# Optimization experiments

Hardware: AMD Instinct MI355X
Metric: run time of the kernel (lower is better)

The kernel has to match this reference:

```python
import jax, jax.numpy as jnp
import numpy as np

B, C, H, W = 4, 256, 64, 64
G = 32          # GroupNorm groups
KH = KW = 3     # deformable kernel
K = KH * KW
EPS = 1e-5
PAD = 1
DIL = 1
STRIDE = 1


def conv3x3(x, w, b):
    # plain 3x3 conv, stride 1, pad 1 (offset-prediction conv)
    y = jax.lax.conv_general_dilated(
        x, w, window_strides=(1, 1), padding=((1, 1), (1, 1)),
        dimension_numbers=('NCHW', 'OIHW', 'NCHW'))
    return y + b[None, :, None, None]


def group_norm(x, gamma, beta):
    b, c, h, w = x.shape
    xr = x.reshape(b, G, -1)
    mu = jnp.mean(xr, axis=-1, keepdims=True)
    var = jnp.var(xr, axis=-1, keepdims=True)
    xn = ((xr - mu) * jax.lax.rsqrt(var + EPS)).reshape(b, c, h, w)
    return xn * gamma[None, :, None, None] + beta[None, :, None, None]


def deform_conv(x, offset, weight):
    # x: [B,Cin,H,W]; offset: [B,2*K,H,W] as (dy,dx) pairs per kernel tap;
    # weight: [Cout,Cin,KH,KW]. DeformConv v1, no bias, stride=1, pad=1.
    b, cin, h, w = x.shape
    cout = weight.shape[0]
    off = offset.reshape(b, K, 2, h, w)
    dy, dx = off[:, :, 0], off[:, :, 1]          # [B,K,H,W]

    ky = (jnp.arange(K) // KW).astype(x.dtype)   # kernel tap row
    kx = (jnp.arange(K) % KW).astype(x.dtype)    # kernel tap col
    hh = jnp.arange(h, dtype=x.dtype)
    ww = jnp.arange(w, dtype=x.dtype)

    # fractional sampling coordinates, shape [B,K,H,W]
    py = dy + hh[None, None, :, None] * STRIDE - PAD + ky[None, :, None, None] * DIL
    px = dx + ww[None, None, None, :] * STRIDE - PAD + kx[None, :, None, None] * DIL

    y0 = jnp.floor(py)
    x0 = jnp.floor(px)
    ly = py - y0   # bilinear fractions
    lx = px - x0

    xf = x.reshape(b, cin, h * w)

    def gather(yi, xi):
        valid = ((yi >= 0) & (yi < h) & (xi >= 0) & (xi < w)).astype(x.dtype)
        yc = jnp.clip(yi, 0, h - 1).astype(jnp.int32)
        xc = jnp.clip(xi, 0, w - 1).astype(jnp.int32)
        idx = (yc * w + xc).reshape(b, 1, K * h * w)
        g = jnp.take_along_axis(xf, idx, axis=2).reshape(b, cin, K, h, w)
        return g * valid[:, None]

    # accumulate 4 bilinear corners -> sampled patches [B,Cin,K,H,W]
    val = gather(y0, x0) * ((1 - ly) * (1 - lx))[:, None]
    val = val + gather(y0, x0 + 1) * ((1 - ly) * lx)[:, None]
    val = val + gather(y0 + 1, x0) * (ly * (1 - lx))[:, None]
    val = val + gather(y0 + 1, x0 + 1) * (ly * lx)[:, None]

    wk = weight.reshape(cout, cin, K)
    return jnp.einsum('bckhw,ock->bohw', val, wk)


def setup_inputs() -> dict:
    key = jax.random.key(0)
    ks = jax.random.split(key, 12)
    fan = 1.0 / np.sqrt(C * K)
    off_scale = 0.01  # small offsets -> near-grid sampling, as after training-time zero-init
    return {
        'x':      jax.random.normal(ks[0], (B, C, H, W), jnp.float32),
        'w_off1': jax.random.normal(ks[1], (2 * K, C, KH, KW), jnp.float32) * off_scale,
        'b_off1': jnp.zeros((2 * K,), jnp.float32),
        'w_off2': jax.random.normal(ks[2], (2 * K, C, KH, KW), jnp.float32) * off_scale,
        'b_off2': jnp.zeros((2 * K,), jnp.float32),
        'w_def1': jax.random.normal(ks[3], (C, C, KH, KW), jnp.float32) * fan,
        'w_def2': jax.random.normal(ks[4], (C, C, KH, KW), jnp.float32) * fan,
        'gamma1': jnp.ones((C,), jnp.float32),
        'beta1':  jnp.zeros((C,), jnp.float32),
        'gamma2': jnp.ones((C,), jnp.float32),
        'beta2':  jnp.zeros((C,), jnp.float32),
    }


def reference(x, w_off1, b_off1, w_off2, b_off2, w_def1, w_def2,
              gamma1, beta1, gamma2, beta2):
    residual = x
    offset = conv3x3(x, w_off1, b_off1)
    out = deform_conv(x, offset, w_def1)
    out = jax.nn.relu(group_norm(out, gamma1, beta1))
    offset2 = conv3x3(out, w_off2, b_off2)
    out = deform_conv(out, offset2, w_def2)
    out = group_norm(out, gamma2, beta2)
    out = jax.nn.relu(out + residual)
    return out
```

## Files before the change

### kernel.cpp

```cpp
#include <hip/hip_runtime.h>
#include <hip/hip_bf16.h>

typedef unsigned int uint;
typedef unsigned short ushort;
typedef __attribute__((ext_vector_type(8))) short bfrag_t;
typedef __attribute__((ext_vector_type(4))) short s4_t;
typedef __attribute__((ext_vector_type(4))) float f4_t;
typedef __attribute__((ext_vector_type(2))) float f2_t;

#define EPSV 1e-5f

__device__ __forceinline__ float4 ld4(const float* p) { return *(const float4*)p; }
__device__ __forceinline__ void st4(float* p, float4 v) { *(float4*)p = v; }

__device__ __forceinline__ ushort f2bf(float f) {
    union { float f; uint u; } v; v.f = f;
    uint r = v.u + 0x7fffu + ((v.u >> 16) & 1u);
    return (ushort)(r >> 16);
}
__device__ __forceinline__ float bf2f(ushort s) {
    union { uint u; float f; } v; v.u = ((uint)s) << 16;
    return v.f;
}
__device__ __forceinline__ float bfhi(uint u) { union { uint u; float f; } v; v.u = u & 0xffff0000u; return v.f; }
__device__ __forceinline__ float bflo(uint u) { union { uint u; float f; } v; v.u = u << 16; return v.f; }
__device__ __forceinline__ uint pk2(float a, float b) { return (uint)f2bf(a) | ((uint)f2bf(b) << 16); }
__device__ __forceinline__ uint pkrn(float a, float b) {
    union { __hip_bfloat162 h; uint u; } v;
    v.h = __float22bfloat162_rn(make_float2(a, b));
    return v.u;
}

__global__ __launch_bounds__(256) void prep_all(const float* __restrict__ wd1, const float* __restrict__ wd2,
                                                const float* __restrict__ wo1, const float* __restrict__ wo2,
                                                const float* __restrict__ x,
                                                ushort* __restrict__ oT1, ushort* __restrict__ oT2,
                                                ushort* __restrict__ oO1, ushort* __restrict__ oO2,
                                                ushort* __restrict__ xb, float* __restrict__ gnacc) {
    __shared__ float lds[64][65];
    int bid = blockIdx.x;
    int tid = threadIdx.x;
    if (bid < 512) {
        int co = bid & 255;
        int sel = bid >> 8;
        const float* w = sel ? wd2 : wd1;
        ushort* o = sel ? oT2 : oT1;
        const float* p = w + (co * 256 + tid) * 9;
        float v[9];
#pragma unroll
        for (int k = 0; k < 9; ++k) v[k] = p[k];
#pragma unroll
        for (int k = 0; k < 9; ++k) o[(k * 256 + co) * 256 + tid] = f2bf(v[k]);
    } else if (bid < 576) {
        int idx = bid - 512;
        int co = idx & 31;
        int sel = idx >> 5;
        const float* w = sel ? wo2 : wo1;
        ushort* o = sel ? oO2 : oO1;
        float v[9] = {0.f,0.f,0.f,0.f,0.f,0.f,0.f,0.f,0.f};
        if (co < 18) {
            const float* p = w + (co * 256 + tid) * 9;
#pragma unroll
            for (int k = 0; k < 9; ++k) v[k] = p[k];
        }
#pragma unroll
        for (int k = 0; k < 9; ++k) o[(k * 32 + co) * 256 + tid] = f2bf(v[k]);
        if (idx == 0) { gnacc[tid] = 0.f; gnacc[256 + tid] = 0.f; }
    } else {
        int b2 = bid - 576;
        int cb = b2 & 3, y = (b2 >> 2) & 63, b = b2 >> 8;
        int c0 = cb << 6;
#pragma unroll
        for (int i = 0; i < 4; ++i) {
            int q = tid + (i << 8);
            int c_l = q >> 4, x4 = (q & 15) << 2;
            float4 v = ld4(&x[((b * 256 + c0 + c_l) << 12) + (y << 6) + x4]);
            lds[c_l][x4 + 0] = v.x; lds[c_l][x4 + 1] = v.y; lds[c_l][x4 + 2] = v.z; lds[c_l][x4 + 3] = v.w;
        }
        __syncthreads();
#pragma unroll
        for (int i = 0; i < 4; ++i) {
            int q = tid + (i << 8);
            int x_l = q >> 4, c4 = (q & 15) << 2;
            s4_t v;
            v.x = (short)f2bf(lds[c4 + 0][x_l]); v.y = (short)f2bf(lds[c4 + 1][x_l]);
            v.z = (short)f2bf(lds[c4 + 2][x_l]); v.w = (short)f2bf(lds[c4 + 3][x_l]);
            *(s4_t*)&xb[(((b << 12) + (y << 6) + x_l) << 8) + c0 + c4] = v;
        }
    }
}

template<int FUSE>
__global__ __launch_bounds__(512, 2) void offconv8(const ushort* __restrict__ xb, const float* __restrict__ gnacc,
                                                   const float* __restrict__ gamma, const float* __restrict__ beta,
                                                   const ushort* __restrict__ wO,
                                                   const float* __restrict__ bias, float* __restrict__ offb) {
    __shared__ float red2[8][64][33];
    int bidx = blockIdx.x;
    int tile = (bidx & 7) * 32 + (bidx >> 3);
    int px0 = tile << 6;
    int b = tile >> 6;
    int y = tile & 63;
    int tid = threadIdx.x;
    int wave = tid >> 6, lane = tid & 63;
    int lr = lane & 15, lq = lane >> 4;
    int cio = (wave << 5) + (lq << 3);

    float s8[8], t8[8];
    if (FUSE) {
        int g = cio >> 3;
        float2 a = *(const float2*)(gnacc + ((b << 5) + g) * 2);
        float mean = a.x * (1.f / 32768.f);
        float var = fmaxf(a.y * (1.f / 32768.f) - mean * mean, 0.f);
        float rstd = rsqrtf(var + EPSV);
#pragma unroll
        for (int j = 0; j < 8; ++j) {
            float ga = gamma[cio + j];
            s8[j] = ga * rstd;
            t8[j] = beta[cio + j] - mean * s8[j];
        }
    }

    f4_t acc[4][2];
#pragma unroll
    for (int m = 0; m < 4; ++m)
#pragma unroll
        for (int n = 0; n < 2; ++n) acc[m][n] = (f4_t){0.f,0.f,0.f,0.f};

#pragma unroll
    for (int tap = 0; tap < 9; ++tap) {
        int ky = tap / 3, kx = tap - ky * 3;
        int yy = y + ky - 1;
        if ((uint)yy < 64u) {
            const ushort* wrow = wO + ((tap << 5) << 8) + cio;
            bfrag_t b0 = *(const bfrag_t*)(wrow + (lr << 8));
            bfrag_t b1 = *(const bfrag_t*)(wrow + ((16 + lr) << 8));
            const ushort* arow = xb + (((b << 6) + yy) << 14) + cio;
#pragma unroll
            for (int m = 0; m < 4; ++m) {
                int xx = (m << 4) + lr + kx - 1;
                bfrag_t afr = (bfrag_t){0,0,0,0,0,0,0,0};
                if ((uint)xx < 64u) {
                    if (FUSE) {
                        uint4 raw = *(const uint4*)(arow + (xx << 8));
                        union { uint4 u; bfrag_t f; } cv;
                        cv.u.x = pkrn(fmaxf(s8[0]*bflo(raw.x)+t8[0], 0.f), fmaxf(s8[1]*bfhi(raw.x)+t8[1], 0.f));
                        cv.u.y = pkrn(fmaxf(s8[2]*bflo(raw.y)+t8[2], 0.f), fmaxf(s8[3]*bfhi(raw.y)+t8[3], 0.f));
                        cv.u.z = pkrn(fmaxf(s8[4]*bflo(raw.z)+t8[4], 0.f), fmaxf(s8[5]*bfhi(raw.z)+t8[5], 0.f));
                        cv.u.w = pkrn(fmaxf(s8[6]*bflo(raw.w)+t8[6], 0.f), fmaxf(s8[7]*bfhi(raw.w)+t8[7], 0.f));
                        afr = cv.f;
                    } else {
                        afr = *(const bfrag_t*)(arow + (xx << 8));
                    }
                }
                acc[m][0] = __builtin_amdgcn_mfma_f32_16x16x32_bf16(afr, b0, acc[m][0], 0, 0, 0);
                acc[m][1] = __builtin_amdgcn_mfma_f32_16x16x32_bf16(afr, b1, acc[m][1], 0, 0, 0);
            }
        }
    }
#pragma unroll
    for (int m = 0; m < 4; ++m)
#pragma unroll
        for (int n = 0; n < 2; ++n)
#pragma unroll
            for (int r = 0; r < 4; ++r)
                red2[wave][lane][(m << 3) + (n << 2) + r] = acc[m][n][r];
    __syncthreads();
#pragma unroll
    for (int e = 0; e < 4; ++e) {
        int oi = tid + (e << 9);
        int px = oi >> 5, co = oi & 31;
        int m = px >> 4, w4 = px & 15;
        int lanes = ((w4 >> 2) << 4) + (co & 15);
        int elem = (m << 3) + ((co >> 4) << 2) + (w4 & 3);
        float v = 0.f;
#pragma unroll
        for (int w = 0; w < 8; ++w) v += red2[w][lanes][elem];
        if (co < 18) offb[(px0 + px) * 18 + co] = v + bias[co];
    }
}

template<int FUSE>
__global__ __launch_bounds__(512, 2) void deform_mfma(const ushort* __restrict__ xb, const float* __restrict__ gnin,
                                                      const float* __restrict__ gamma, const float* __restrict__ beta,
                                                      const float* __restrict__ offb,
                                                      const ushort* __restrict__ wT, ushort* __restrict__ outb,
                                                      float* __restrict__ gnacc) {
    __shared__ short As[2][16384];
    __shared__ float red[64];

    int bidx = blockIdx.x;
    int tile = (bidx & 7) * 32 + (bidx >> 3);
    int px0 = tile << 6;
    int bb = px0 >> 12;

    int tid = threadIdx.x;
    int wave = tid >> 6;
    int lane = tid & 63;
    int lr = lane & 15, lq = lane >> 4;

    if (tid < 64) red[tid] = 0.f;

    int gpx = tid >> 3;
    int gl = tid & 7;
    int pxg = px0 + gpx;
    int gy = (pxg >> 6) & 63, gx = pxg & 63;
    int gbase = (pxg >> 12) << 12;
    const float* offp = offb + pxg * 18;

    f2_t s2[4][4], t2[4][4];
    if (FUSE) {
#pragma unroll
        for (int u = 0; u < 4; ++u) {
            int g = (u << 3) + gl;
            float2 a = *(const float2*)(gnin + ((bb << 5) + g) * 2);
            float mean = a.x * (1.f / 32768.f);
            float var = fmaxf(a.y * (1.f / 32768.f) - mean * mean, 0.f);
            float rstd = rsqrtf(var + EPSV);
            int c0 = (u << 6) + (gl << 3);
            float4 ga0 = ld4(&gamma[c0]), ga1 = ld4(&gamma[c0 + 4]);
            float4 be0 = ld4(&beta[c0]),  be1 = ld4(&beta[c0 + 4]);
            s2[u][0] = (f2_t){ga0.x * rstd, ga0.y * rstd};
            s2[u][1] = (f2_t){ga0.z * rstd, ga0.w * rstd};
            s2[u][2] = (f2_t){ga1.x * rstd, ga1.y * rstd};
            s2[u][3] = (f2_t){ga1.z * rstd, ga1.w * rstd};
            t2[u][0] = (f2_t){be0.x - mean * s2[u][0].x, be0.y - mean * s2[u][0].y};
            t2[u][1] = (f2_t){be0.z - mean * s2[u][1].x, be0.w - mean * s2[u][1].y};
            t2[u][2] = (f2_t){be1.x - mean * s2[u][2].x, be1.y - mean * s2[u][2].y};
            t2[u][3] = (f2_t){be1.z - mean * s2[u][3].x, be1.w - mean * s2[u][3].y};
        }
    }

    f4_t acc[4][2];
#pragma unroll
    for (int m = 0; m < 4; ++m)
#pragma unroll
        for (int n = 0; n < 2; ++n) acc[m][n] = (f4_t){0.f,0.f,0.f,0.f};

    uint4 q[4][4];
    float cw0, cw1, cw2, cw3;

    auto gload = [&](int tap) {
        int ky = tap / 3, kx = tap - ky * 3;
        float2 of = *(const float2*)(offp + 2 * tap);
        float py  = of.x + (float)(gy - 1 + ky);
        float pxx = of.y + (float)(gx - 1 + kx);
        float y0f = floorf(py), x0f = floorf(pxx);
        float ly = py - y0f, lx = pxx - x0f;
        int y0 = (int)y0f, x0 = (int)x0f;
        int y1 = y0 + 1, x1 = x0 + 1;
        float wy0 = ((uint)y0 < 64u) ? (1.f - ly) : 0.f;
        float wy1 = ((uint)y1 < 64u) ? ly : 0.f;
        float wx0 = ((uint)x0 < 64u) ? (1.f - lx) : 0.f;
        float wx1 = ((uint)x1 < 64u) ? lx : 0.f;
        int y0c = min(max(y0, 0), 63), y1c = min(max(y1, 0), 63);
        int x0c = min(max(x0, 0), 63), x1c = min(max(x1, 0), 63);
        cw0 = wy0 * wx0; cw1 = wy0 * wx1; cw2 = wy1 * wx0; cw3 = wy1 * wx1;
        const ushort* s0 = xb + ((gbase + (y0c << 6) + x0c) << 8) + (gl << 3);
        const ushort* s1 = xb + ((gbase + (y0c << 6) + x1c) << 8) + (gl << 3);
        const ushort* s2p = xb + ((gbase + (y1c << 6) + x0c) << 8) + (gl << 3);
        const ushort* s3 = xb + ((gbase + (y1c << 6) + x1c) << 8) + (gl << 3);
#pragma unroll
        for (int u = 0; u < 4; ++u) {
            q[0][u] = *(const uint4*)(s0 + (u << 6));
            q[1][u] = *(const uint4*)(s1 + (u << 6));
            q[2][u] = *(const uint4*)(s2p + (u << 6));
            q[3][u] = *(const uint4*)(s3 + (u << 6));
        }
    };

    auto gstore = [&](int buf) {
        f2_t w0 = {cw0, cw0}, w1 = {cw1, cw1}, w2 = {cw2, cw2}, w3 = {cw3, cw3};
#pragma unroll
        for (int u = 0; u < 4; ++u) {
            uint4 q0 = q[0][u], q1 = q[1][u], q2 = q[2][u], q3 = q[3][u];
            auto nrm = [&](uint w, int j) -> f2_t {
                f2_t v = (f2_t){bflo(w), bfhi(w)};
                if (FUSE) {
                    v = s2[u][j] * v + t2[u][j];
                    v.x = fmaxf(v.x, 0.f);
                    v.y = fmaxf(v.y, 0.f);
                }
                return v;
            };
            f2_t a0 = w0 * nrm(q0.x,0) + w1 * nrm(q1.x,0) + w2 * nrm(q2.x,0) + w3 * nrm(q3.x,0);
            f2_t a1 = w0 * nrm(q0.y,1) + w1 * nrm(q1.y,1) + w2 * nrm(q2.y,1) + w3 * nrm(q3.y,1);
            f2_t a2 = w0 * nrm(q0.z,2) + w1 * nrm(q1.z,2) + w2 * nrm(q2.z,2) + w3 * nrm(q3.z,2);
            f2_t a3 = w0 * nrm(q0.w,3) + w1 * nrm(q1.w,3) + w2 * nrm(q2.w,3) + w3 * nrm(q3.w,3);
            uint4 o;
            o.x = pkrn(a0.x, a0.y); o.y = pkrn(a1.x, a1.y);
            o.z = pkrn(a2.x, a2.y); o.w = pkrn(a3.x, a3.y);
            int kblk = (u << 3) + gl;
            int chunk = (kblk << 6) + (gpx ^ (kblk & 7));
            *(uint4*)&As[buf][chunk << 3] = o;
        }
    };

    auto gemm = [&](int tap, int buf) {
        const ushort* wbase = wT + ((tap << 8) + (wave << 5) + lr) * 256 + (lq << 3);
        bfrag_t bf0[8], bf1[8];
#pragma unroll
        for (int s = 0; s < 8; ++s) {
            bf0[s] = *(const bfrag_t*)(wbase + (s << 5));
            bf1[s] = *(const bfrag_t*)(wbase + (16 << 8) + (s << 5));
        }
#pragma unroll
        for (int s = 0; s < 8; ++s) {
            int kblk = (s << 2) + lq;
            int kx7 = kblk & 7;
#pragma unroll
            for (int m = 0; m < 4; ++m) {
                int chunk = (kblk << 6) + (((m << 4) + lr) ^ kx7);
                bfrag_t a = *(const bfrag_t*)&As[buf][chunk << 3];
                acc[m][0] = __builtin_amdgcn_mfma_f32_16x16x32_bf16(a, bf0[s], acc[m][0], 0, 0, 0);
                acc[m][1] = __builtin_amdgcn_mfma_f32_16x16x32_bf16(a, bf1[s], acc[m][1], 0, 0, 0);
            }
        }
    };

    gload(0);
    gstore(0);
    __syncthreads();
    for (int tap = 0; tap < 9; ++tap) {
        if (tap < 8) gload(tap + 1);
        gemm(tap, tap & 1);
        if (tap < 8) gstore((tap + 1) & 1);
        __syncthreads();
    }

    int cob = wave << 5;
#pragma unroll
    for (int n = 0; n < 2; ++n) {
        int co = cob + (n << 4) + lr;
        float s = 0.f, s2v = 0.f;
#pragma unroll
        for (int m = 0; m < 4; ++m)
#pragma unroll
            for (int r = 0; r < 4; ++r) {
                float v = acc[m][n][r];
                s += v; s2v += v * v;
                As[0][(((m << 4) + (lq << 2) + r) << 8) + co] = (short)f2bf(v);
            }
        int g = co >> 3;
        atomicAdd(&red[g], s);
        atomicAdd(&red[32 + g], s2v);
    }
    __syncthreads();
    {
        const uint4* src = (const uint4*)&As[0][0];
        uint4* dst = (uint4*)&outb[px0 << 8];
#pragma unroll
        for (int i = 0; i < 4; ++i)
            dst[tid + (i << 9)] = src[tid + (i << 9)];
    }
    if (tid < 32) {
        atomicAdd(&gnacc[((bb << 5) + tid) * 2], red[tid]);
        atomicAdd(&gnacc[((bb << 5) + tid) * 2 + 1], red[32 + tid]);
    }
}

__global__ __launch_bounds__(256) void final_bf16(const ushort* __restrict__ v2, const float* __restrict__ gnacc,
                                                  const float* __restrict__ gamma, const float* __restrict__ beta,
                                                  const float* __restrict__ xin, float* __restrict__ out) {
    __shared__ float lds[64][65];
    int bid = blockIdx.x;
    int cb = bid & 3, y = (bid >> 2) & 63, b = bid >> 8;
    int c0 = cb << 6;
    int tid = threadIdx.x;
#pragma unroll
    for (int i = 0; i < 4; ++i) {
        int q = tid + (i << 8);
        int x_l = q >> 4, c4 = (q & 15) << 2;
        s4_t v = *(const s4_t*)&v2[(((b << 12) + (y << 6) + x_l) << 8) + c0 + c4];
        lds[c4 + 0][x_l] = bf2f((ushort)v.x); lds[c4 + 1][x_l] = bf2f((ushort)v.y);
        lds[c4 + 2][x_l] = bf2f((ushort)v.z); lds[c4 + 3][x_l] = bf2f((ushort)v.w);
    }
    __syncthreads();
#pragma unroll
    for (int i = 0; i < 4; ++i) {
        int q = tid + (i << 8);
        int c_l = q >> 4, x4 = (q & 15) << 2;
        int c = c0 + c_l;
        int g = c >> 3;
        float2 a = *(const float2*)(gnacc + ((b << 5) + g) * 2);
        float mean = a.x * (1.f / 32768.f);
        float var = fmaxf(a.y * (1.f / 32768.f) - mean * mean, 0.f);
        float rstd = rsqrtf(var + EPSV);
        float ga = gamma[c], be = beta[c];
        const float* xp = &xin[((b << 8) + c) * 4096 + (y << 6) + x4];
        float4 r = ld4(xp);
        float4 o;
        o.x = fmaxf((lds[c_l][x4 + 0] - mean) * rstd * ga + be + r.x, 0.f);
        o.y = fmaxf((lds[c_l][x4 + 1] - mean) * rstd * ga + be + r.y, 0.f);
        o.z = fmaxf((lds[c_l][x4 + 2] - mean) * rstd * ga + be + r.z, 0.f);
        o.w = fmaxf((lds[c_l][x4 + 3] - mean) * rstd * ga + be + r.w, 0.f);
        st4(&out[((b << 8) + c) * 4096 + (y << 6) + x4], o);
    }
}

extern "C" void kernel_launch(void* const* d_in, const int* in_sizes, int n_in,
                              void* d_out, int out_size, void* d_ws, size_t ws_size,
                              hipStream_t stream) {
    (void)in_sizes; (void)n_in; (void)out_size; (void)ws_size;
    const float* x      = (const float*)d_in[0];
    const float* w_off1 = (const float*)d_in[1];
    const float* b_off1 = (const float*)d_in[2];
    const float* w_off2 = (const float*)d_in[3];
    const float* b_off2 = (const float*)d_in[4];
    const float* w_def1 = (const float*)d_in[5];
    const float* w_def2 = (const float*)d_in[6];
    const float* gamma1 = (const float*)d_in[7];
    const float* beta1  = (const float*)d_in[8];
    const float* gamma2 = (const float*)d_in[9];
    const float* beta2  = (const float*)d_in[10];
    float* out = (float*)d_out;

    float* ws = (float*)d_ws;
    float*  xb_f   = ws;
    float*  xb2_f  = xb_f + 2097152;
    float*  wT1_f  = xb2_f + 2097152;
    float*  wT2_f  = wT1_f + 294912;
    float*  wO1_f  = wT2_f + 294912;
    float*  wO2_f  = wO1_f + 36864;
    float*  offb   = wO2_f + 36864;
    float*  gnacc1 = offb + 294912;
    float*  gnacc2 = gnacc1 + 256;

    ushort* xb  = (ushort*)xb_f;
    ushort* v2b = (ushort*)xb_f;
    ushort* wT1 = (ushort*)wT1_f;
    ushort* wT2 = (ushort*)wT2_f;
    ushort* wO1 = (ushort*)wO1_f;
    ushort* wO2 = (ushort*)wO2_f;
    ushort* t1b = (ushort*)d_out;

    prep_all<<<1600, 256, 0, stream>>>(w_def1, w_def2, w_off1, w_off2, x,
                                       wT1, wT2, wO1, wO2, xb, gnacc1);
    offconv8<0><<<256, 512, 0, stream>>>(xb, nullptr, nullptr, nullptr, wO1, b_off1, offb);
    deform_mfma<0><<<256, 512, 0, stream>>>(xb, nullptr, nullptr, nullptr, offb, wT1, t1b, gnacc1);
    offconv8<1><<<256, 512, 0, stream>>>(t1b, gnacc1, gamma1, beta1, wO2, b_off2, offb);
    deform_mfma<1><<<256, 512, 0, stream>>>(t1b, gnacc1, gamma1, beta1, offb, wT2, v2b, gnacc2);
    final_bf16<<<1024, 256, 0, stream>>>(v2b, gnacc2, gamma2, beta2, x, out);
}
```

Before: 243.9 us.

## Fuse offset conv into deformable conv kernel, keep offsets in LDS

Merges the offset-prediction 3x3 conv and the deformable conv into one kernel per stage. Each block computes the offsets for its 64-pixel row into shared memory and consumes them directly, so the global offset buffer and two launches go away. The reduction scratch space is aliased with the A-tile buffers in one shared pool. This cuts launch overhead and the offset round trip through global memory. The trade-off is more serialized work per block and a different LDS footprint, which may affect occupancy.

Measured after the change: 241.1 us. About the same (-1.2%).

```diff
diff --git a/kernel.cpp b/kernel.cpp
--- a/kernel.cpp
+++ b/kernel.cpp
@@ -91,122 +91,113 @@
 }
 
 template<int FUSE>
-__global__ __launch_bounds__(512, 2) void offconv8(const ushort* __restrict__ xb, const float* __restrict__ gnacc,
-                                                   const float* __restrict__ gamma, const float* __restrict__ beta,
-                                                   const ushort* __restrict__ wO,
-                                                   const float* __restrict__ bias, float* __restrict__ offb) {
-    __shared__ float red2[8][64][33];
+__global__ __launch_bounds__(512, 2) void stage(const ushort* __restrict__ xb, const float* __restrict__ gnin,
+                                                const float* __restrict__ gamma, const float* __restrict__ beta,
+                                                const ushort* __restrict__ wO, const float* __restrict__ obias,
+                                                const ushort* __restrict__ wT, ushort* __restrict__ outb,
+                                                float* __restrict__ gnacc) {
+    __shared__ __align__(16) char pool[8 * 64 * 33 * 4];
+    __shared__ float offs[64][18];
+    __shared__ float red[64];
+
+    typedef float Red2Row[64][33];
+    Red2Row* red2 = (Red2Row*)pool;
+    short (*As)[16384] = (short(*)[16384])pool;
+
     int bidx = blockIdx.x;
     int tile = (bidx & 7) * 32 + (bidx >> 3);
     int px0 = tile << 6;
     int b = tile >> 6;
     int y = tile & 63;
+    int bb = b;
+
     int tid = threadIdx.x;
     int wave = tid >> 6, lane = tid & 63;
     int lr = lane & 15, lq = lane >> 4;
-    int cio = (wave << 5) + (lq << 3);
-
-    float s8[8], t8[8];
-    if (FUSE) {
-        int g = cio >> 3;
-        float2 a = *(const float2*)(gnacc + ((b << 5) + g) * 2);
-        float mean = a.x * (1.f / 32768.f);
-        float var = fmaxf(a.y * (1.f / 32768.f) - mean * mean, 0.f);
-        float rstd = rsqrtf(var + EPSV);
-#pragma unroll
-        for (int j = 0; j < 8; ++j) {
-            float ga = gamma[cio + j];
-            s8[j] = ga * rstd;
-            t8[j] = beta[cio + j] - mean * s8[j];
-        }
-    }
-
-    f4_t acc[4][2];
-#pragma unroll
-    for (int m = 0; m < 4; ++m)
-#pragma unroll
-        for (int n = 0; n < 2; ++n) acc[m][n] = (f4_t){0.f,0.f,0.f,0.f};
-
-#pragma unroll
-    for (int tap = 0; tap < 9; ++tap) {
-        int ky = tap / 3, kx = tap - ky * 3;
-        int yy = y + ky - 1;
-        if ((uint)yy < 64u) {
-            const ushort* wrow = wO + ((tap << 5) << 8) + cio;
-            bfrag_t b0 = *(const bfrag_t*)(wrow + (lr << 8));
-            bfrag_t b1 = *(const bfrag_t*)(wrow + ((16 + lr) << 8));
-            const ushort* arow = xb + (((b << 6) + yy) << 14) + cio;
-#pragma unroll
-            for (int m = 0; m < 4; ++m) {
-                int xx = (m << 4) + lr + kx - 1;
-                bfrag_t afr = (bfrag_t){0,0,0,0,0,0,0,0};
-                if ((uint)xx < 64u) {
-                    if (FUSE) {
-                        uint4 raw = *(const uint4*)(arow + (xx << 8));
-                        union { uint4 u; bfrag_t f; } cv;
-                        cv.u.x = pkrn(fmaxf(s8[0]*bflo(raw.x)+t8[0], 0.f), fmaxf(s8[1]*bfhi(raw.x)+t8[1], 0.f));
-                        cv.u.y = pkrn(fmaxf(s8[2]*bflo(raw.y)+t8[2], 0.f), fmaxf(s8[3]*bfhi(raw.y)+t8[3], 0.f));
-                        cv.u.z = pkrn(fmaxf(s8[4]*bflo(raw.z)+t8[4], 0.f), fmaxf(s8[5]*bfhi(raw.z)+t8[5], 0.f));
-                        cv.u.w = pkrn(fmaxf(s8[6]*bflo(raw.w)+t8[6], 0.f), fmaxf(s8[7]*bfhi(raw.w)+t8[7], 0.f));
-                        afr = cv.f;
-                    } else {
-                        afr = *(const bfrag_t*)(arow + (xx << 8));
+
+    {
+        int cio = (wave << 5) + (lq << 3);
+
+        float s8[8], t8[8];
+        if (FUSE) {
+            int g = cio >> 3;
+            float2 a = *(const float2*)(gnin + ((b << 5) + g) * 2);
+            float mean = a.x * (1.f / 32768.f);
+            float var = fmaxf(a.y * (1.f / 32768.f) - mean * mean, 0.f);
+            float rstd = rsqrtf(var + EPSV);
+#pragma unroll
+            for (int j = 0; j < 8; ++j) {
+                s8[j] = gamma[cio + j] * rstd;
+                t8[j] = beta[cio + j] - mean * s8[j];
+            }
+        }
+
+        f4_t acc[4][2];
+#pragma unroll
+        for (int m = 0; m < 4; ++m)
+#pragma unroll
+            for (int n = 0; n < 2; ++n) acc[m][n] = (f4_t){0.f,0.f,0.f,0.f};
+
+#pragma unroll
+        for (int tap = 0; tap < 9; ++tap) {
+            int ky = tap / 3, kx = tap - ky * 3;
+            int yy = y + ky - 1;
+            if ((uint)yy < 64u) {
+                const ushort* wrow = wO + ((tap << 5) << 8) + cio;
+                bfrag_t b0 = *(const bfrag_t*)(wrow + (lr << 8));
+                bfrag_t b1 = *(const bfrag_t*)(wrow + ((16 + lr) << 8));
+                const ushort* arow = xb + (((b << 6) + yy) << 14) + cio;
+#pragma unroll
+                for (int m = 0; m < 4; ++m) {
+                    int xx = (m << 4) + lr + kx - 1;
+                    bfrag_t afr = (bfrag_t){0,0,0,0,0,0,0,0};
+                    if ((uint)xx < 64u) {
+                        if (FUSE) {
+                            uint4 raw = *(const uint4*)(arow + (xx << 8));
+                            union { uint4 u; bfrag_t f; } cv;
+                            cv.u.x = pkrn(fmaxf(s8[0]*bflo(raw.x)+t8[0], 0.f), fmaxf(s8[1]*bfhi(raw.x)+t8[1], 0.f));
+                            cv.u.y = pkrn(fmaxf(s8[2]*bflo(raw.y)+t8[2], 0.f), fmaxf(s8[3]*bfhi(raw.y)+t8[3], 0.f));
+                            cv.u.z = pkrn(fmaxf(s8[4]*bflo(raw.z)+t8[4], 0.f), fmaxf(s8[5]*bfhi(raw.z)+t8[5], 0.f));
+                            cv.u.w = pkrn(fmaxf(s8[6]*bflo(raw.w)+t8[6], 0.f), fmaxf(s8[7]*bfhi(raw.w)+t8[7], 0.f));
+                            afr = cv.f;
+                        } else {
+                            afr = *(const bfrag_t*)(arow + (xx << 8));
+                        }
                     }
+                    acc[m][0] = __builtin_amdgcn_mfma_f32_16x16x32_bf16(afr, b0, acc[m][0], 0, 0, 0);
+                    acc[m][1] = __builtin_amdgcn_mfma_f32_16x16x32_bf16(afr, b1, acc[m][1], 0, 0, 0);
                 }
-                acc[m][0] = __builtin_amdgcn_mfma_f32_16x16x32_bf16(afr, b0, acc[m][0], 0, 0, 0);
-                acc[m][1] = __builtin_amdgcn_mfma_f32_16x16x32_bf16(afr, b1, acc[m][1], 0, 0, 0);
             }
         }
-    }
-#pragma unroll
-    for (int m = 0; m < 4; ++m)
-#pragma unroll
-        for (int n = 0; n < 2; ++n)
-#pragma unroll
-            for (int r = 0; r < 4; ++r)
-                red2[wave][lane][(m << 3) + (n << 2) + r] = acc[m][n][r];
-    __syncthreads();
-#pragma unroll
-    for (int e = 0; e < 4; ++e) {
-        int oi = tid + (e << 9);
-        int px = oi >> 5, co = oi & 31;
-        int m = px >> 4, w4 = px & 15;
-        int lanes = ((w4 >> 2) << 4) + (co & 15);
-        int elem = (m << 3) + ((co >> 4) << 2) + (w4 & 3);
-        float v = 0.f;
-#pragma unroll
-        for (int w = 0; w < 8; ++w) v += red2[w][lanes][elem];
-        if (co < 18) offb[(px0 + px) * 18 + co] = v + bias[co];
-    }
-}
-
-template<int FUSE>
-__global__ __launch_bounds__(512, 2) void deform_mfma(const ushort* __restrict__ xb, const float* __restrict__ gnin,
-                                                      const float* __restrict__ gamma, const float* __restrict__ beta,
-                                                      const float* __restrict__ offb,
-                                                      const ushort* __restrict__ wT, ushort* __restrict__ outb,
-                                                      float* __restrict__ gnacc) {
-    __shared__ short As[2][16384];
-    __shared__ float red[64];
-
-    int bidx = blockIdx.x;
-    int tile = (bidx & 7) * 32 + (bidx >> 3);
-    int px0 = tile << 6;
-    int bb = px0 >> 12;
-
-    int tid = threadIdx.x;
-    int wave = tid >> 6;
-    int lane = tid & 63;
-    int lr = lane & 15, lq = lane >> 4;
-
-    if (tid < 64) red[tid] = 0.f;
+#pragma unroll
+        for (int m = 0; m < 4; ++m)
+#pragma unroll
+            for (int n = 0; n < 2; ++n)
+#pragma unroll
+                for (int r = 0; r < 4; ++r)
+                    red2[wave][lane][(m << 3) + (n << 2) + r] = acc[m][n][r];
+        __syncthreads();
+#pragma unroll
+        for (int e = 0; e < 4; ++e) {
+            int oi = tid + (e << 9);
+            int px = oi >> 5, co = oi & 31;
+            int m = px >> 4, w4 = px & 15;
+            int lanes = ((w4 >> 2) << 4) + (co & 15);
+            int elem = (m << 3) + ((co >> 4) << 2) + (w4 & 3);
+            float v = 0.f;
+#pragma unroll
+            for (int w = 0; w < 8; ++w) v += red2[w][lanes][elem];
+            if (co < 18) offs[px][co] = v + obias[co];
+        }
+        if (tid < 64) red[tid] = 0.f;
+        __syncthreads();
+    }
 
     int gpx = tid >> 3;
     int gl = tid & 7;
     int pxg = px0 + gpx;
     int gy = (pxg >> 6) & 63, gx = pxg & 63;
     int gbase = (pxg >> 12) << 12;
-    const float* offp = offb + pxg * 18;
 
     f2_t s2[4][4], t2[4][4];
     if (FUSE) {
@@ -242,7 +233,7 @@
 
     auto gload = [&](int tap) {
         int ky = tap / 3, kx = tap - ky * 3;
-        float2 of = *(const float2*)(offp + 2 * tap);
+        float2 of = *(const float2*)&offs[gpx][2 * tap];
         float py  = of.x + (float)(gy - 1 + ky);
         float pxx = of.y + (float)(gx - 1 + kx);
         float y0f = floorf(py), x0f = floorf(pxx);
@@ -256,16 +247,16 @@
         int y0c = min(max(y0, 0), 63), y1c = min(max(y1, 0), 63);
         int x0c = min(max(x0, 0), 63), x1c = min(max(x1, 0), 63);
         cw0 = wy0 * wx0; cw1 = wy0 * wx1; cw2 = wy1 * wx0; cw3 = wy1 * wx1;
-        const ushort* s0 = xb + ((gbase + (y0c << 6) + x0c) << 8) + (gl << 3);
-        const ushort* s1 = xb + ((gbase + (y0c << 6) + x1c) << 8) + (gl << 3);
-        const ushort* s2p = xb + ((gbase + (y1c << 6) + x0c) << 8) + (gl << 3);
-        const ushort* s3 = xb + ((gbase + (y1c << 6) + x1c) << 8) + (gl << 3);
+        const ushort* p0 = xb + ((gbase + (y0c << 6) + x0c) << 8) + (gl << 3);
+        const ushort* p1 = xb + ((gbase + (y0c << 6) + x1c) << 8) + (gl << 3);
+        const ushort* p2 = xb + ((gbase + (y1c << 6) + x0c) << 8) + (gl << 3);
+        const ushort* p3 = xb + ((gbase + (y1c << 6) + x1c) << 8) + (gl << 3);
 #pragma unroll
         for (int u = 0; u < 4; ++u) {
-            q[0][u] = *(const uint4*)(s0 + (u << 6));
-            q[1][u] = *(const uint4*)(s1 + (u << 6));
-            q[2][u] = *(const uint4*)(s2p + (u << 6));
-            q[3][u] = *(const uint4*)(s3 + (u << 6));
+            q[0][u] = *(const uint4*)(p0 + (u << 6));
+            q[1][u] = *(const uint4*)(p1 + (u << 6));
+            q[2][u] = *(const uint4*)(p2 + (u << 6));
+            q[3][u] = *(const uint4*)(p3 + (u << 6));
         }
     };
 
@@ -436,9 +427,7 @@
 
     prep_all<<<1600, 256, 0, stream>>>(w_def1, w_def2, w_off1, w_off2, x,
                                        wT1, wT2, wO1, wO2, xb, gnacc1);
-    offconv8<0><<<256, 512, 0, stream>>>(xb, nullptr, nullptr, nullptr, wO1, b_off1, offb);
-    deform_mfma<0><<<256, 512, 0, stream>>>(xb, nullptr, nullptr, nullptr, offb, wT1, t1b, gnacc1);
-    offconv8<1><<<256, 512, 0, stream>>>(t1b, gnacc1, gamma1, beta1, wO2, b_off2, offb);
-    deform_mfma<1><<<256, 512, 0, stream>>>(t1b, gnacc1, gamma1, beta1, offb, wT2, v2b, gnacc2);
+    stage<0><<<256, 512, 0, stream>>>(xb, nullptr, nullptr, nullptr, wO1, b_off1, wT1, t1b, gnacc1);
+    stage<1><<<256, 512, 0, stream>>>(t1b, gnacc1, gamma1, beta1, wO2, b_off2, wT2, v2b, gnacc2);
     final_bf16<<<1024, 256, 0, stream>>>(v2b, gnacc2, gamma2, beta2, x, out);
 }
```
